# Kernel optimization log

Hardware: AMD Instinct MI355X
Metric: run time of the kernel (lower is better)

The kernel has to match this reference:

```python
import jax, jax.numpy as jnp
import numpy as np

N, IN, D, H = 65536, 512, 256, 4  # nodes, in_channels, out_channels (per head), num_heads


def setup_inputs() -> dict:
    key = jax.random.key(0)
    ks = jax.random.split(key, 8)
    s = 1.0 / np.sqrt(IN)  # torch nn.Linear default init range
    def lin(kw, kb):
        W = jax.random.uniform(kw, (IN, H * D), jnp.float32, -s, s)
        b = jax.random.uniform(kb, (H * D,), jnp.float32, -s, s)
        return W, b
    Wq, bq = lin(ks[0], ks[1])
    Wk, bk = lin(ks[2], ks[3])
    Wv, bv = lin(ks[4], ks[5])
    x = jax.random.normal(ks[6], (N, IN), jnp.float32)
    n_nodes = jnp.array([N], jnp.int32)  # single graph; unused when block_wise=False
    return {"x": x, "Wq": Wq, "bq": bq, "Wk": Wk, "bk": bk, "Wv": Wv, "bv": bv,
            "n_nodes": n_nodes}


def reference(x, Wq, bq, Wk, bk, Wv, bv, n_nodes):
    # Projections -> [N, H, D]
    q = (x @ Wq + bq).reshape(N, H, D)
    k = (x @ Wk + bk).reshape(N, H, D)
    v = (x @ Wv + bv).reshape(N, H, D)
    # L2-normalize q, k per head (kernel='simple')
    qn = q / jnp.linalg.norm(q, axis=-1, keepdims=True)
    kn = k / jnp.linalg.norm(k, axis=-1, keepdims=True)
    # Linear attention: K^T V then Q @ (KV), all heads at once
    kv = jnp.einsum('nhm,nhd->hmd', kn, v)                    # [H, D, D]
    num = jnp.einsum('nhm,hmd->nhd', qn, kv) + v.sum(axis=0)  # [N, H, D]
    ksum = kn.sum(axis=0)                                     # [H, D]
    denom = jnp.einsum('nhm,hm->nh', qn, ksum) + jnp.float32(N)  # [N, H]
    out = num / denom[..., None]
    return out.mean(axis=1)  # mean over heads -> [N, D]
```

## Files before the change

### kernel.cpp

```cpp
#include <hip/hip_runtime.h>

#define NNODES 65536
#define INC    512
#define NH     4
#define HD     256
#define HDTOT  1024

typedef __bf16 bf16_t;
typedef __bf16 bf16x4_t __attribute__((ext_vector_type(4)));
typedef __bf16 bf16x8_t __attribute__((ext_vector_type(8)));
typedef float  f32x4_t  __attribute__((ext_vector_type(4)));

__device__ __forceinline__ bf16_t f2bf(float f) { return (bf16_t)f; }

__device__ __forceinline__ void gl_lds16(const void* g, void* l) {
  __builtin_amdgcn_global_load_lds(
      (const __attribute__((address_space(1))) void*)g,
      (__attribute__((address_space(3))) void*)l, 16, 0, 0);
}

__global__ void k0_wt(const float* __restrict__ Wq, const float* __restrict__ Wk,
                      const float* __restrict__ Wv, bf16_t* __restrict__ Wt) {
  __shared__ float tile[32][33];
  int mat = blockIdx.z;
  const float* W = (mat == 0) ? Wq : (mat == 1) ? Wk : Wv;
  int n0 = blockIdx.x * 32, k0 = blockIdx.y * 32;
  int t = threadIdx.x, tc = t & 31, tr = t >> 5;
#pragma unroll
  for (int i = 0; i < 4; ++i)
    tile[tr + i * 8][tc] = W[(size_t)(k0 + tr + i * 8) * HDTOT + n0 + tc];
  __syncthreads();
#pragma unroll
  for (int i = 0; i < 4; ++i)
    Wt[((size_t)mat * HDTOT + n0 + tr + i * 8) * INC + k0 + tc] =
        f2bf(tile[tc][tr + i * 8]);
}

__global__ void k0b_xb(const float* __restrict__ x, bf16_t* __restrict__ xb) {
  size_t i = ((size_t)blockIdx.x * 256 + threadIdx.x) * 8;
  float4 a = *(const float4*)(x + i);
  float4 b = *(const float4*)(x + i + 4);
  bf16x8_t o;
  o[0] = f2bf(a.x); o[1] = f2bf(a.y); o[2] = f2bf(a.z); o[3] = f2bf(a.w);
  o[4] = f2bf(b.x); o[5] = f2bf(b.y); o[6] = f2bf(b.z); o[7] = f2bf(b.w);
  *(bf16x8_t*)(xb + i) = o;
}

__global__ __launch_bounds__(512, 4) void k1_qkv(
    const bf16_t* __restrict__ xb, const bf16_t* __restrict__ Wt,
    const float* __restrict__ bq, const float* __restrict__ bk,
    const float* __restrict__ bv,
    bf16_t* __restrict__ qn, bf16_t* __restrict__ knT, bf16_t* __restrict__ vT,
    float* __restrict__ ksum, float* __restrict__ vsum) {
  __shared__ __align__(16) char smem[52224];
  char* la = smem;
  char* lb = smem + 16384;
  bf16_t* ept = (bf16_t*)smem;
  float* sred  = (float*)(smem + 49152);
  float* sredc = (float*)(smem + 51200);

  const int gxy = blockIdx.x;
  const int mat = gxy >> 2, head = gxy & 3;
  const int n0 = blockIdx.y * 128;
  const int t = threadIdx.x;
  const int wid = t >> 6, lane = t & 63;
  const int l15 = lane & 15, l4 = lane >> 4;
  const int wr = wid >> 2, wc = wid & 3;

  const f32x4_t zero4 = {0.f, 0.f, 0.f, 0.f};
  f32x4_t acc[4][4];
#pragma unroll
  for (int i = 0; i < 4; ++i)
#pragma unroll
    for (int j = 0; j < 4; ++j) acc[i][j] = zero4;

  const char* Ab = (const char*)(xb + (size_t)n0 * INC);
  const char* Bb = (const char*)(Wt + ((size_t)mat * HDTOT + head * HD) * INC);

  for (int kc = 0; kc < 8; ++kc) {
    const int kb = kc * 128;
#pragma unroll
    for (int i = 0; i < 2; ++i) {
      int ow = i * 8192 + wid * 1024;
      int o = ow + lane * 16;
      gl_lds16(Ab + (size_t)(o >> 7) * 1024 + kb + (o & 127), la + ow);
    }
#pragma unroll
    for (int i = 0; i < 4; ++i) {
      int ow = i * 8192 + wid * 1024;
      int o = ow + lane * 16;
      gl_lds16(Bb + (size_t)(o >> 7) * 1024 + kb + (o & 127), lb + ow);
    }
    __syncthreads();
#pragma unroll
    for (int ks = 0; ks < 2; ++ks) {
      const int cc = ks * 64 + l4 * 16;
      bf16x8_t af[4], bfr[4];
#pragma unroll
      for (int i = 0; i < 4; ++i)
        af[i] = *(const bf16x8_t*)(la + (wr * 64 + i * 16 + l15) * 128 + cc);
#pragma unroll
      for (int j = 0; j < 4; ++j)
        bfr[j] = *(const bf16x8_t*)(lb + (wc * 64 + j * 16 + l15) * 128 + cc);
#pragma unroll
      for (int i = 0; i < 4; ++i)
#pragma unroll
        for (int j = 0; j < 4; ++j)
          acc[i][j] = __builtin_amdgcn_mfma_f32_16x16x32_bf16(af[i], bfr[j], acc[i][j], 0, 0, 0);
    }
    __syncthreads();
  }

  const float* bias = (mat == 0) ? bq : (mat == 1) ? bk : bv;
#pragma unroll
  for (int jf = 0; jf < 4; ++jf) {
    float bb = bias[head * HD + wc * 64 + jf * 16 + l15];
#pragma unroll
    for (int i = 0; i < 4; ++i)
#pragma unroll
      for (int jj = 0; jj < 4; ++jj) acc[i][jf][jj] += bb;
  }

  if (mat <= 1) {
    float ss[4][4];
#pragma unroll
    for (int i = 0; i < 4; ++i)
#pragma unroll
      for (int jj = 0; jj < 4; ++jj) {
        float s = 0.f;
#pragma unroll
        for (int jf = 0; jf < 4; ++jf) s += acc[i][jf][jj] * acc[i][jf][jj];
        ss[i][jj] = s;
      }
#pragma unroll
    for (int off = 1; off < 16; off <<= 1)
#pragma unroll
      for (int i = 0; i < 4; ++i)
#pragma unroll
        for (int jj = 0; jj < 4; ++jj) ss[i][jj] += __shfl_xor(ss[i][jj], off, 64);
    if (l15 == 0) {
#pragma unroll
      for (int i = 0; i < 4; ++i)
#pragma unroll
        for (int jj = 0; jj < 4; ++jj)
          sred[(wr * 64 + i * 16 + l4 * 4 + jj) * 4 + wc] = ss[i][jj];
    }
    __syncthreads();
#pragma unroll
    for (int i = 0; i < 4; ++i)
#pragma unroll
      for (int jj = 0; jj < 4; ++jj) {
        int row = wr * 64 + i * 16 + l4 * 4 + jj;
        float s = sred[row * 4] + sred[row * 4 + 1] + sred[row * 4 + 2] + sred[row * 4 + 3];
        float rn = rsqrtf(s);
#pragma unroll
        for (int jf = 0; jf < 4; ++jf) acc[i][jf][jj] *= rn;
      }
  }

  if (mat >= 1) {
    float cs[4];
#pragma unroll
    for (int jf = 0; jf < 4; ++jf) {
      float s = 0.f;
#pragma unroll
      for (int i = 0; i < 4; ++i)
#pragma unroll
        for (int jj = 0; jj < 4; ++jj) s += acc[i][jf][jj];
      s += __shfl_xor(s, 16, 64);
      s += __shfl_xor(s, 32, 64);
      cs[jf] = s;
    }
    if (t < 256) sredc[t] = 0.f;
    __syncthreads();
    if (l4 == 0) {
#pragma unroll
      for (int jf = 0; jf < 4; ++jf)
        atomicAdd(&sredc[wc * 64 + jf * 16 + l15], cs[jf]);
    }
    __syncthreads();
    float* dstSum = (mat == 1) ? ksum : vsum;
    if (t < 256) atomicAdd(dstSum + head * HD + t, sredc[t]);
  }

  const int ldp = (mat == 0) ? 264 : 258;
  for (int ph = 0; ph < 2; ++ph) {
    __syncthreads();
    if (wr == ph) {
#pragma unroll
      for (int i = 0; i < 4; ++i)
#pragma unroll
        for (int jf = 0; jf < 4; ++jf)
#pragma unroll
          for (int jj = 0; jj < 4; ++jj)
            ept[(i * 16 + l4 * 4 + jj) * ldp + wc * 64 + jf * 16 + l15] =
                f2bf(acc[i][jf][jj]);
    }
    __syncthreads();
    const int hn0 = n0 + ph * 64;
    if (mat == 0) {
#pragma unroll
      for (int i = 0; i < 4; ++i) {
        int idx = t + i * 512;
        int r = idx >> 5, c8 = (idx & 31) * 8;
        *(bf16x8_t*)(qn + (size_t)(hn0 + r) * HDTOT + head * HD + c8) =
            *(const bf16x8_t*)(ept + r * 264 + c8);
      }
    } else {
      int m = t & 255, seg = t >> 8;
      bf16_t* dst = (mat == 1) ? knT : vT;
      unsigned int pack[16];
#pragma unroll
      for (int rr = 0; rr < 32; rr += 2) {
        int r = seg * 32 + rr;
        unsigned int a = *(const unsigned short*)(ept + r * 258 + m);
        unsigned int b = *(const unsigned short*)(ept + (r + 1) * 258 + m);
        pack[rr >> 1] = a | (b << 16);
      }
      uint4* dp = (uint4*)(dst + ((size_t)head * HD + m) * NNODES + hn0 + seg * 32);
#pragma unroll
      for (int i = 0; i < 4; ++i)
        dp[i] = make_uint4(pack[i * 4], pack[i * 4 + 1], pack[i * 4 + 2], pack[i * 4 + 3]);
    }
  }
}

__global__ __launch_bounds__(256, 4) void k2_kv(
    const bf16_t* __restrict__ knT, const bf16_t* __restrict__ vT,
    float* __restrict__ kvT) {
  __shared__ __align__(16) char smem[32768];
  char* la = smem;
  char* lb = smem + 16384;

  const int gx = blockIdx.x;
  const int head = blockIdx.y, chunk = blockIdx.z;
  const int td = gx >> 1, tm = gx & 1;
  const int d0 = td * 128, m0 = tm * 128;

  const int t = threadIdx.x, wid = t >> 6, lane = t & 63;
  const int l15 = lane & 15, l4 = lane >> 4;
  const int wr = wid >> 1, wc = wid & 1;

  const f32x4_t zero4 = {0.f, 0.f, 0.f, 0.f};
  f32x4_t acc[4][4];
#pragma unroll
  for (int i = 0; i < 4; ++i)
#pragma unroll
    for (int j = 0; j < 4; ++j) acc[i][j] = zero4;

  const char* As = (const char*)vT  + ((size_t)head * HD + d0) * (NNODES * 2) + (size_t)chunk * 8192;
  const char* Bs = (const char*)knT + ((size_t)head * HD + m0) * (NNODES * 2) + (size_t)chunk * 8192;

  for (int c = 0; c < 64; ++c) {
    const int kb = c * 128;
#pragma unroll
    for (int i = 0; i < 4; ++i) {
      int ow = i * 4096 + wid * 1024;
      int o = ow + lane * 16;
      int r = o >> 7, cb = o & 127;
      gl_lds16(As + (size_t)r * (NNODES * 2) + kb + cb, la + ow);
      gl_lds16(Bs + (size_t)r * (NNODES * 2) + kb + cb, lb + ow);
    }
    __syncthreads();
#pragma unroll
    for (int ks = 0; ks < 2; ++ks) {
      const int cc = ks * 64 + l4 * 16;
      bf16x8_t af[4], bfr[4];
#pragma unroll
      for (int i = 0; i < 4; ++i)
        af[i] = *(const bf16x8_t*)(la + (wr * 64 + i * 16 + l15) * 128 + cc);
#pragma unroll
      for (int j = 0; j < 4; ++j)
        bfr[j] = *(const bf16x8_t*)(lb + (wc * 64 + j * 16 + l15) * 128 + cc);
#pragma unroll
      for (int i = 0; i < 4; ++i)
#pragma unroll
        for (int j = 0; j < 4; ++j)
          acc[i][j] = __builtin_amdgcn_mfma_f32_16x16x32_bf16(af[i], bfr[j], acc[i][j], 0, 0, 0);
    }
    __syncthreads();
  }

#pragma unroll
  for (int i = 0; i < 4; ++i)
#pragma unroll
    for (int jj = 0; jj < 4; ++jj)
#pragma unroll
      for (int j = 0; j < 4; ++j) {
        int d = d0 + wr * 64 + i * 16 + l4 * 4 + j;
        int m = m0 + wc * 64 + jj * 16 + l15;
        atomicAdd(&kvT[((size_t)head * HD + d) * HD + m], acc[i][jj][j]);
      }
}

__global__ void k3_cvt(const float* __restrict__ kvT, bf16_t* __restrict__ kvTb) {
  int i = blockIdx.x * 256 + threadIdx.x;
  float4 v = *(const float4*)(kvT + (size_t)i * 4);
  bf16x4_t b;
  b[0] = f2bf(v.x); b[1] = f2bf(v.y); b[2] = f2bf(v.z); b[3] = f2bf(v.w);
  *(bf16x4_t*)(kvTb + (size_t)i * 4) = b;
}

__global__ __launch_bounds__(256) void k4_out(
    const bf16_t* __restrict__ qn, const bf16_t* __restrict__ kvTb,
    const float* __restrict__ ksum, const float* __restrict__ vsum,
    float* __restrict__ out) {
  __shared__ __align__(16) bf16_t la[64 * 72];
  __shared__ __align__(16) bf16_t lb[256 * 72];
  __shared__ float sdn[256];

  const int n0 = blockIdx.x * 64;
  const int t = threadIdx.x, wid = t >> 6, lane = t & 63;
  const int l15 = lane & 15, l4 = lane >> 4;

  const f32x4_t zero4 = {0.f, 0.f, 0.f, 0.f};
  f32x4_t oacc[16];
#pragma unroll
  for (int f = 0; f < 16; ++f) oacc[f] = zero4;

  for (int h = 0; h < NH; ++h) {
    f32x4_t hacc[16];
#pragma unroll
    for (int f = 0; f < 16; ++f) hacc[f] = zero4;
    float dnp = 0.f;

    for (int mc = 0; mc < 4; ++mc) {
      const int m0 = mc * 64;
#pragma unroll
      for (int i = 0; i < 2; ++i) {
        int idx = t + i * 256;
        int r = idx >> 3, c8 = (idx & 7) * 8;
        *(bf16x8_t*)(la + r * 72 + c8) =
            *(const bf16x8_t*)(qn + (size_t)(n0 + r) * HDTOT + h * HD + m0 + c8);
      }
#pragma unroll
      for (int i = 0; i < 8; ++i) {
        int idx = t + i * 256;
        int r = idx >> 3, c8 = (idx & 7) * 8;
        *(bf16x8_t*)(lb + r * 72 + c8) =
            *(const bf16x8_t*)(kvTb + ((size_t)h * HD + r) * HD + m0 + c8);
      }
      __syncthreads();
      {
        int r = t & 63, qd = t >> 6;
        float s = 0.f;
#pragma unroll
        for (int j = 0; j < 16; ++j)
          s += (float)la[r * 72 + qd * 16 + j] * ksum[h * HD + m0 + qd * 16 + j];
        dnp += s;
      }
#pragma unroll
      for (int ks = 0; ks < 2; ++ks) {
        const int kk = ks * 32 + l4 * 8;
        bf16x8_t af = *(const bf16x8_t*)(la + (wid * 16 + l15) * 72 + kk);
#pragma unroll
        for (int f = 0; f < 16; ++f) {
          bf16x8_t bf_ = *(const bf16x8_t*)(lb + (f * 16 + l15) * 72 + kk);
          hacc[f] = __builtin_amdgcn_mfma_f32_16x16x32_bf16(af, bf_, hacc[f], 0, 0, 0);
        }
      }
      __syncthreads();
    }
    sdn[t] = dnp;
    __syncthreads();
    if (t < 64) {
      float dn = sdn[t] + sdn[t + 64] + sdn[t + 128] + sdn[t + 192] + 65536.0f;
      sdn[t] = 1.0f / dn;
    }
    __syncthreads();
    float rdn[4];
#pragma unroll
    for (int j = 0; j < 4; ++j) rdn[j] = sdn[wid * 16 + l4 * 4 + j];
#pragma unroll
    for (int f = 0; f < 16; ++f) {
      float vs = vsum[h * HD + f * 16 + l15];
#pragma unroll
      for (int j = 0; j < 4; ++j) oacc[f][j] += (hacc[f][j] + vs) * rdn[j];
    }
    __syncthreads();
  }
#pragma unroll
  for (int f = 0; f < 16; ++f)
#pragma unroll
    for (int j = 0; j < 4; ++j)
      out[(size_t)(n0 + wid * 16 + l4 * 4 + j) * HD + f * 16 + l15] =
          oacc[f][j] * 0.25f;
}

extern "C" void kernel_launch(void* const* d_in, const int* in_sizes, int n_in,
                              void* d_out, int out_size, void* d_ws, size_t ws_size,
                              hipStream_t stream) {
  const float* x  = (const float*)d_in[0];
  const float* Wq = (const float*)d_in[1];
  const float* bq = (const float*)d_in[2];
  const float* Wk = (const float*)d_in[3];
  const float* bk = (const float*)d_in[4];
  const float* Wv = (const float*)d_in[5];
  const float* bv = (const float*)d_in[6];
  float* out = (float*)d_out;
  char* ws = (char*)d_ws;

  bf16_t* qn   = (bf16_t*)(ws);
  bf16_t* knT  = (bf16_t*)(ws + 134217728L);
  bf16_t* vT   = (bf16_t*)(ws + 268435456L);
  bf16_t* Wt   = (bf16_t*)(ws + 402653184L);
  float*  kvT  = (float*) (ws + 405798912L);
  bf16_t* kvTb = (bf16_t*)(ws + 406847488L);
  float*  ksum = (float*) (ws + 407371776L);
  float*  vsum = (float*) (ws + 407375872L);
  bf16_t* xb   = (bf16_t*)(ws + 407379968L);

  hipMemsetAsync(kvT, 0, 1048576, stream);
  hipMemsetAsync(ksum, 0, 8192, stream);

  k0_wt  <<<dim3(32, 16, 3), 256, 0, stream>>>(Wq, Wk, Wv, Wt);
  k0b_xb <<<dim3(16384),     256, 0, stream>>>(x, xb);
  k1_qkv <<<dim3(12, 512),   512, 0, stream>>>(xb, Wt, bq, bk, bv, qn, knT, vT, ksum, vsum);
  k2_kv  <<<dim3(4, 4, 16),  256, 0, stream>>>(knT, vT, kvT);
  k3_cvt <<<dim3(256),       256, 0, stream>>>(kvT, kvTb);
  k4_out <<<dim3(1024),      256, 0, stream>>>(qn, kvTb, ksum, vsum, out);
}
```

Baseline: 822.8 us.

## Double-buffer GEMM loads, swizzle LDS, tile K/V layout, replace atomics with partial reduction

The QKV projection and KV GEMM kernels now double-buffer their LDS tiles so global-to-LDS loads for the next k-step overlap with MFMA work. LDS rows use an XOR swizzle to avoid bank conflicts, and MFMA regions are raised in priority. K and V are written in a blocked 64-node tile layout so the KV kernel reads contiguous 16 KB chunks. Float atomics into kvT are replaced by per-chunk partial buffers summed in a separate reduction kernel, which removes the memset. The output kernel loads a full Q head row block at once via direct LDS loads and computes the denominator in one pass. The partial buffer reuses the xb workspace region, which is safe only because xb is dead by the time it is written. The changes also add LDS pressure, which could reduce occupancy.

```diff
diff --git a/kernel.cpp b/kernel.cpp
--- a/kernel.cpp
+++ b/kernel.cpp
@@ -50,12 +50,10 @@
     const bf16_t* __restrict__ xb, const bf16_t* __restrict__ Wt,
     const float* __restrict__ bq, const float* __restrict__ bk,
     const float* __restrict__ bv,
-    bf16_t* __restrict__ qn, bf16_t* __restrict__ knT, bf16_t* __restrict__ vT,
+    bf16_t* __restrict__ qn, bf16_t* __restrict__ knT2, bf16_t* __restrict__ vT2,
     float* __restrict__ ksum, float* __restrict__ vsum) {
   __shared__ __align__(16) char smem[52224];
-  char* la = smem;
-  char* lb = smem + 16384;
-  bf16_t* ept = (bf16_t*)smem;
+  bf16_t* ept  = (bf16_t*)smem;
   float* sred  = (float*)(smem + 49152);
   float* sredc = (float*)(smem + 51200);
 
@@ -77,38 +75,47 @@
   const char* Ab = (const char*)(xb + (size_t)n0 * INC);
   const char* Bb = (const char*)(Wt + ((size_t)mat * HDTOT + head * HD) * INC);
 
-  for (int kc = 0; kc < 8; ++kc) {
-    const int kb = kc * 128;
+  auto stage = [&](int kt, int c) {
+    const int kb = kt * 64;
+    {
+      int o = t * 16, r = o >> 6, cb = o & 63;
+      gl_lds16(Ab + (size_t)r * 1024 + kb + (cb ^ ((r & 3) << 4)), smem + c * 8192 + o);
+    }
 #pragma unroll
     for (int i = 0; i < 2; ++i) {
-      int ow = i * 8192 + wid * 1024;
-      int o = ow + lane * 16;
-      gl_lds16(Ab + (size_t)(o >> 7) * 1024 + kb + (o & 127), la + ow);
-    }
+      int o = i * 8192 + t * 16, r = o >> 6, cb = o & 63;
+      gl_lds16(Bb + (size_t)r * 1024 + kb + (cb ^ ((r & 3) << 4)),
+               smem + 16384 + c * 16384 + o);
+    }
+  };
+
+  stage(0, 0);
+  __syncthreads();
+  int cur = 0;
+  for (int kt = 0; kt < 16; ++kt) {
+    if (kt < 15) stage(kt + 1, cur ^ 1);
+    const char* lA = smem + cur * 8192;
+    const char* lB = smem + 16384 + cur * 16384;
+    bf16x8_t af[4], bfr[4];
 #pragma unroll
     for (int i = 0; i < 4; ++i) {
-      int ow = i * 8192 + wid * 1024;
-      int o = ow + lane * 16;
-      gl_lds16(Bb + (size_t)(o >> 7) * 1024 + kb + (o & 127), lb + ow);
-    }
-    __syncthreads();
-#pragma unroll
-    for (int ks = 0; ks < 2; ++ks) {
-      const int cc = ks * 64 + l4 * 16;
-      bf16x8_t af[4], bfr[4];
-#pragma unroll
-      for (int i = 0; i < 4; ++i)
-        af[i] = *(const bf16x8_t*)(la + (wr * 64 + i * 16 + l15) * 128 + cc);
+      int r = wr * 64 + i * 16 + l15;
+      af[i] = *(const bf16x8_t*)(lA + r * 64 + ((l4 * 16) ^ ((r & 3) << 4)));
+    }
+#pragma unroll
+    for (int j = 0; j < 4; ++j) {
+      int r = wc * 64 + j * 16 + l15;
+      bfr[j] = *(const bf16x8_t*)(lB + r * 64 + ((l4 * 16) ^ ((r & 3) << 4)));
+    }
+    __builtin_amdgcn_s_setprio(1);
+#pragma unroll
+    for (int i = 0; i < 4; ++i)
 #pragma unroll
       for (int j = 0; j < 4; ++j)
-        bfr[j] = *(const bf16x8_t*)(lb + (wc * 64 + j * 16 + l15) * 128 + cc);
-#pragma unroll
-      for (int i = 0; i < 4; ++i)
-#pragma unroll
-        for (int j = 0; j < 4; ++j)
-          acc[i][j] = __builtin_amdgcn_mfma_f32_16x16x32_bf16(af[i], bfr[j], acc[i][j], 0, 0, 0);
-    }
-    __syncthreads();
+        acc[i][j] = __builtin_amdgcn_mfma_f32_16x16x32_bf16(af[i], bfr[j], acc[i][j], 0, 0, 0);
+    __builtin_amdgcn_s_setprio(0);
+    __syncthreads();
+    cur ^= 1;
   }
 
   const float* bias = (mat == 0) ? bq : (mat == 1) ? bk : bv;
@@ -208,7 +215,7 @@
       }
     } else {
       int m = t & 255, seg = t >> 8;
-      bf16_t* dst = (mat == 1) ? knT : vT;
+      bf16_t* dst = (mat == 1) ? knT2 : vT2;
       unsigned int pack[16];
 #pragma unroll
       for (int rr = 0; rr < 32; rr += 2) {
@@ -217,7 +224,9 @@
         unsigned int b = *(const unsigned short*)(ept + (r + 1) * 258 + m);
         pack[rr >> 1] = a | (b << 16);
       }
-      uint4* dp = (uint4*)(dst + ((size_t)head * HD + m) * NNODES + hn0 + seg * 32);
+      size_t base = ((((size_t)(head * 2 + (m >> 7)) * 1024 + (hn0 >> 6)) * 128 +
+                      (m & 127)) * 64) + seg * 32;
+      uint4* dp = (uint4*)(dst + base);
 #pragma unroll
       for (int i = 0; i < 4; ++i)
         dp[i] = make_uint4(pack[i * 4], pack[i * 4 + 1], pack[i * 4 + 2], pack[i * 4 + 3]);
@@ -226,16 +235,13 @@
 }
 
 __global__ __launch_bounds__(256, 4) void k2_kv(
-    const bf16_t* __restrict__ knT, const bf16_t* __restrict__ vT,
-    float* __restrict__ kvT) {
-  __shared__ __align__(16) char smem[32768];
-  char* la = smem;
-  char* lb = smem + 16384;
+    const bf16_t* __restrict__ knT2, const bf16_t* __restrict__ vT2,
+    float* __restrict__ kvP) {
+  __shared__ __align__(16) char smem[65536];
 
   const int gx = blockIdx.x;
-  const int head = blockIdx.y, chunk = blockIdx.z;
+  const int head = blockIdx.y, ch = blockIdx.z;
   const int td = gx >> 1, tm = gx & 1;
-  const int d0 = td * 128, m0 = tm * 128;
 
   const int t = threadIdx.x, wid = t >> 6, lane = t & 63;
   const int l15 = lane & 15, l4 = lane >> 4;
@@ -248,66 +254,83 @@
 #pragma unroll
     for (int j = 0; j < 4; ++j) acc[i][j] = zero4;
 
-  const char* As = (const char*)vT  + ((size_t)head * HD + d0) * (NNODES * 2) + (size_t)chunk * 8192;
-  const char* Bs = (const char*)knT + ((size_t)head * HD + m0) * (NNODES * 2) + (size_t)chunk * 8192;
-
-  for (int c = 0; c < 64; ++c) {
-    const int kb = c * 128;
+  const char* Abase = (const char*)vT2  + ((size_t)(head * 2 + td) * 1024 + ch * 32) * 16384;
+  const char* Bbase = (const char*)knT2 + ((size_t)(head * 2 + tm) * 1024 + ch * 32) * 16384;
+
+  auto stage = [&](int it, int c) {
 #pragma unroll
     for (int i = 0; i < 4; ++i) {
-      int ow = i * 4096 + wid * 1024;
-      int o = ow + lane * 16;
-      int r = o >> 7, cb = o & 127;
-      gl_lds16(As + (size_t)r * (NNODES * 2) + kb + cb, la + ow);
-      gl_lds16(Bs + (size_t)r * (NNODES * 2) + kb + cb, lb + ow);
-    }
-    __syncthreads();
+      int o = i * 4096 + t * 16, r = o >> 7, cb = o & 127;
+      int so = r * 128 + (cb ^ ((r & 7) << 4));
+      gl_lds16(Abase + (size_t)it * 16384 + so, smem + c * 16384 + o);
+      gl_lds16(Bbase + (size_t)it * 16384 + so, smem + 32768 + c * 16384 + o);
+    }
+  };
+
+  stage(0, 0);
+  __syncthreads();
+  int cur = 0;
+  for (int it = 0; it < 32; ++it) {
+    if (it < 31) stage(it + 1, cur ^ 1);
+    const char* lA = smem + cur * 16384;
+    const char* lB = smem + 32768 + cur * 16384;
 #pragma unroll
     for (int ks = 0; ks < 2; ++ks) {
-      const int cc = ks * 64 + l4 * 16;
       bf16x8_t af[4], bfr[4];
 #pragma unroll
-      for (int i = 0; i < 4; ++i)
-        af[i] = *(const bf16x8_t*)(la + (wr * 64 + i * 16 + l15) * 128 + cc);
-#pragma unroll
-      for (int j = 0; j < 4; ++j)
-        bfr[j] = *(const bf16x8_t*)(lb + (wc * 64 + j * 16 + l15) * 128 + cc);
+      for (int i = 0; i < 4; ++i) {
+        int r = wr * 64 + i * 16 + l15;
+        af[i] = *(const bf16x8_t*)(lA + r * 128 + ((ks * 64 + l4 * 16) ^ ((r & 7) << 4)));
+      }
+#pragma unroll
+      for (int j = 0; j < 4; ++j) {
+        int r = wc * 64 + j * 16 + l15;
+        bfr[j] = *(const bf16x8_t*)(lB + r * 128 + ((ks * 64 + l4 * 16) ^ ((r & 7) << 4)));
+      }
+      __builtin_amdgcn_s_setprio(1);
 #pragma unroll
       for (int i = 0; i < 4; ++i)
 #pragma unroll
         for (int j = 0; j < 4; ++j)
           acc[i][j] = __builtin_amdgcn_mfma_f32_16x16x32_bf16(af[i], bfr[j], acc[i][j], 0, 0, 0);
-    }
-    __syncthreads();
-  }
-
+      __builtin_amdgcn_s_setprio(0);
+    }
+    __syncthreads();
+    cur ^= 1;
+  }
+
+  float* dst = kvP + ((size_t)(ch * 16 + head * 4 + gx)) * 16384;
 #pragma unroll
   for (int i = 0; i < 4; ++i)
 #pragma unroll
     for (int jj = 0; jj < 4; ++jj)
 #pragma unroll
-      for (int j = 0; j < 4; ++j) {
-        int d = d0 + wr * 64 + i * 16 + l4 * 4 + j;
-        int m = m0 + wc * 64 + jj * 16 + l15;
-        atomicAdd(&kvT[((size_t)head * HD + d) * HD + m], acc[i][jj][j]);
-      }
-}
-
-__global__ void k3_cvt(const float* __restrict__ kvT, bf16_t* __restrict__ kvTb) {
-  int i = blockIdx.x * 256 + threadIdx.x;
-  float4 v = *(const float4*)(kvT + (size_t)i * 4);
+      for (int j = 0; j < 4; ++j)
+        dst[(wr * 64 + i * 16 + l4 * 4 + j) * 128 + wc * 64 + jj * 16 + l15] =
+            acc[i][jj][j];
+}
+
+__global__ void k3_red(const float* __restrict__ kvP, bf16_t* __restrict__ kvTb) {
+  int tid = blockIdx.x * 256 + threadIdx.x;
+  int base = tid * 4;
+  int m = base & 255, d = (base >> 8) & 255, h = base >> 16;
+  int gx = ((d >> 7) << 1) | (m >> 7);
+  int off = (d & 127) * 128 + (m & 127);
+  f32x4_t s = {0.f, 0.f, 0.f, 0.f};
+#pragma unroll
+  for (int ch = 0; ch < 32; ++ch)
+    s += *(const f32x4_t*)(kvP + (((size_t)(ch * 16 + h * 4 + gx)) << 14) + off);
   bf16x4_t b;
-  b[0] = f2bf(v.x); b[1] = f2bf(v.y); b[2] = f2bf(v.z); b[3] = f2bf(v.w);
-  *(bf16x4_t*)(kvTb + (size_t)i * 4) = b;
-}
-
-__global__ __launch_bounds__(256) void k4_out(
+  b[0] = f2bf(s[0]); b[1] = f2bf(s[1]); b[2] = f2bf(s[2]); b[3] = f2bf(s[3]);
+  *(bf16x4_t*)(kvTb + (size_t)base) = b;
+}
+
+__global__ __launch_bounds__(256, 2) void k4_out(
     const bf16_t* __restrict__ qn, const bf16_t* __restrict__ kvTb,
     const float* __restrict__ ksum, const float* __restrict__ vsum,
     float* __restrict__ out) {
-  __shared__ __align__(16) bf16_t la[64 * 72];
-  __shared__ __align__(16) bf16_t lb[256 * 72];
-  __shared__ float sdn[256];
+  __shared__ __align__(16) char smem[66560];
+  float* sdn = (float*)(smem + 65536);
 
   const int n0 = blockIdx.x * 64;
   const int t = threadIdx.x, wid = t >> 6, lane = t & 63;
@@ -318,55 +341,62 @@
 #pragma unroll
   for (int f = 0; f < 16; ++f) oacc[f] = zero4;
 
+  const char* qb  = (const char*)qn + (size_t)n0 * 2048;
+  const char* kvb = (const char*)kvTb;
+
   for (int h = 0; h < NH; ++h) {
+#pragma unroll
+    for (int i = 0; i < 8; ++i) {
+      int o = i * 4096 + t * 16, r = o >> 9, cb = o & 511;
+      int scb = (cb & 0x180) | ((cb & 0x7F) ^ ((r & 7) << 4));
+      gl_lds16(qb + (size_t)r * 2048 + h * 512 + scb, smem + o);
+    }
     f32x4_t hacc[16];
 #pragma unroll
     for (int f = 0; f < 16; ++f) hacc[f] = zero4;
     float dnp = 0.f;
 
     for (int mc = 0; mc < 4; ++mc) {
-      const int m0 = mc * 64;
-#pragma unroll
-      for (int i = 0; i < 2; ++i) {
-        int idx = t + i * 256;
-        int r = idx >> 3, c8 = (idx & 7) * 8;
-        *(bf16x8_t*)(la + r * 72 + c8) =
-            *(const bf16x8_t*)(qn + (size_t)(n0 + r) * HDTOT + h * HD + m0 + c8);
-      }
 #pragma unroll
       for (int i = 0; i < 8; ++i) {
-        int idx = t + i * 256;
-        int r = idx >> 3, c8 = (idx & 7) * 8;
-        *(bf16x8_t*)(lb + r * 72 + c8) =
-            *(const bf16x8_t*)(kvTb + ((size_t)h * HD + r) * HD + m0 + c8);
+        int o = i * 4096 + t * 16, r = o >> 7, cb = o & 127;
+        gl_lds16(kvb + (size_t)h * 131072 + (size_t)r * 512 + mc * 128 +
+                     (cb ^ ((r & 7) << 4)),
+                 smem + 32768 + o);
       }
       __syncthreads();
-      {
+      if (mc == 0) {
         int r = t & 63, qd = t >> 6;
         float s = 0.f;
 #pragma unroll
-        for (int j = 0; j < 16; ++j)
-          s += (float)la[r * 72 + qd * 16 + j] * ksum[h * HD + m0 + qd * 16 + j];
-        dnp += s;
+        for (int j = 0; j < 64; ++j) {
+          int cb2 = (qd * 64 + j) * 2;
+          int a = r * 512 + ((cb2 & 0x180) | ((cb2 & 0x7F) ^ ((r & 7) << 4)));
+          s += (float)(*(const bf16_t*)(smem + a)) * ksum[h * HD + qd * 64 + j];
+        }
+        dnp = s;
       }
 #pragma unroll
       for (int ks = 0; ks < 2; ++ks) {
-        const int kk = ks * 32 + l4 * 8;
-        bf16x8_t af = *(const bf16x8_t*)(la + (wid * 16 + l15) * 72 + kk);
+        int ra = wid * 16 + l15;
+        bf16x8_t af = *(const bf16x8_t*)(
+            smem + ra * 512 + ((mc * 128 + ks * 64 + l4 * 16) ^ ((ra & 7) << 4)));
+        __builtin_amdgcn_s_setprio(1);
 #pragma unroll
         for (int f = 0; f < 16; ++f) {
-          bf16x8_t bf_ = *(const bf16x8_t*)(lb + (f * 16 + l15) * 72 + kk);
-          hacc[f] = __builtin_amdgcn_mfma_f32_16x16x32_bf16(af, bf_, hacc[f], 0, 0, 0);
+          int rb = f * 16 + l15;
+          bf16x8_t bfr = *(const bf16x8_t*)(
+              smem + 32768 + rb * 128 + ((ks * 64 + l4 * 16) ^ ((rb & 7) << 4)));
+          hacc[f] = __builtin_amdgcn_mfma_f32_16x16x32_bf16(af, bfr, hacc[f], 0, 0, 0);
         }
+        __builtin_amdgcn_s_setprio(0);
       }
       __syncthreads();
     }
     sdn[t] = dnp;
     __syncthreads();
-    if (t < 64) {
-      float dn = sdn[t] + sdn[t + 64] + sdn[t + 128] + sdn[t + 192] + 65536.0f;
-      sdn[t] = 1.0f / dn;
-    }
+    if (t < 64)
+      sdn[t] = 1.0f / (sdn[t] + sdn[t + 64] + sdn[t + 128] + sdn[t + 192] + 65536.0f);
     __syncthreads();
     float rdn[4];
 #pragma unroll
@@ -401,22 +431,21 @@
   char* ws = (char*)d_ws;
 
   bf16_t* qn   = (bf16_t*)(ws);
-  bf16_t* knT  = (bf16_t*)(ws + 134217728L);
-  bf16_t* vT   = (bf16_t*)(ws + 268435456L);
+  bf16_t* knT2 = (bf16_t*)(ws + 134217728L);
+  bf16_t* vT2  = (bf16_t*)(ws + 268435456L);
   bf16_t* Wt   = (bf16_t*)(ws + 402653184L);
-  float*  kvT  = (float*) (ws + 405798912L);
   bf16_t* kvTb = (bf16_t*)(ws + 406847488L);
   float*  ksum = (float*) (ws + 407371776L);
   float*  vsum = (float*) (ws + 407375872L);
   bf16_t* xb   = (bf16_t*)(ws + 407379968L);
-
-  hipMemsetAsync(kvT, 0, 1048576, stream);
+  float*  kvP  = (float*) (ws + 407379968L);
+
   hipMemsetAsync(ksum, 0, 8192, stream);
 
   k0_wt  <<<dim3(32, 16, 3), 256, 0, stream>>>(Wq, Wk, Wv, Wt);
   k0b_xb <<<dim3(16384),     256, 0, stream>>>(x, xb);
-  k1_qkv <<<dim3(12, 512),   512, 0, stream>>>(xb, Wt, bq, bk, bv, qn, knT, vT, ksum, vsum);
-  k2_kv  <<<dim3(4, 4, 16),  256, 0, stream>>>(knT, vT, kvT);
-  k3_cvt <<<dim3(256),       256, 0, stream>>>(kvT, kvTb);
+  k1_qkv <<<dim3(12, 512),   512, 0, stream>>>(xb, Wt, bq, bk, bv, qn, knT2, vT2, ksum, vsum);
+  k2_kv  <<<dim3(4, 4, 32),  256, 0, stream>>>(knT2, vT2, kvP);
+  k3_red <<<dim3(256),       256, 0, stream>>>(kvP, kvTb);
   k4_out <<<dim3(1024),      256, 0, stream>>>(qn, kvTb, ksum, vsum, out);
 }
```

Measured after the change: 665.0 us. -19.2%, faster.
